# Kernel tuning notes

Measured on AMD Instinct MI355X. Metric: run time of the kernel, lower is better.

Reference implementation:

```python
import jax, jax.numpy as jnp
import numpy as np


def _block_causal_mask(cu_seqlens, seq_len):
    """Boolean [seq_len, seq_len] mask: True = attend (same doc AND causal)."""
    positions = jnp.arange(seq_len)
    # searchsorted(side='right') - 1 maps each position to its document id
    seq_ids = jnp.searchsorted(cu_seqlens, positions, side='right') - 1
    same_seq = seq_ids[:, None] == seq_ids[None, :]
    causal = positions[None, :] <= positions[:, None]
    return same_seq & causal


def setup_inputs() -> dict:
    key = jax.random.key(0)
    kq, kk, kv, kc = jax.random.split(key, 4)
    B, H, S, D = 1, 16, 4096, 128
    q = jax.random.normal(kq, (B, H, S, D), dtype=jnp.float32)
    k = jax.random.normal(kk, (B, H, S, D), dtype=jnp.float32)
    v = jax.random.normal(kv, (B, H, S, D), dtype=jnp.float32)
    # 8 packed documents: interior boundaries are sorted random ints in (0, S)
    inner = jnp.sort(jax.random.randint(kc, (7,), 1, S, dtype=jnp.int64))
    cu_seqlens = jnp.concatenate([
        jnp.zeros((1,), jnp.int64), inner, jnp.full((1,), S, jnp.int64)
    ])
    return {"q": q, "k": k, "v": v, "cu_seqlens": cu_seqlens, "max_seqlen": S}


def reference(q, k, v, cu_seqlens, max_seqlen):
    # q, k, v: [B, H, S, D]; block-diagonal causal SDPA over packed sequences.
    S, D = q.shape[2], q.shape[3]
    scale = 1.0 / jnp.sqrt(jnp.asarray(D, q.dtype))
    allow = _block_causal_mask(cu_seqlens, S)  # [S, S] bool
    scores = jnp.einsum('bhsd,bhtd->bhst', q, k) * scale  # [B, H, S, S]
    neg_inf = jnp.asarray(-jnp.inf, scores.dtype)
    scores = jnp.where(allow[None, None], scores, neg_inf)
    probs = jax.nn.softmax(scores, axis=-1)
    return jnp.einsum('bhst,bhtd->bhsd', probs, v)
```

## Files before the change

kernel.cpp:

```cpp
#include <hip/hip_runtime.h>

typedef float  f32x4  __attribute__((ext_vector_type(4)));
typedef __bf16 bf16x8 __attribute__((ext_vector_type(8)));
typedef unsigned short u16;
typedef u16 u16x8 __attribute__((ext_vector_type(8)));
typedef u16 u16x4 __attribute__((ext_vector_type(4)));
typedef unsigned u32x4 __attribute__((ext_vector_type(4)));

#define HEADS 16
#define DIM   128
#define QT    64
#define KTILE 64
#define PSTR  72
#define KSTR  136
#define VSTR  68

__device__ __forceinline__ u16 f2bf(float f) {
    unsigned u = __builtin_bit_cast(unsigned, f);
    u += 0x7FFFu + ((u >> 16) & 1u);
    return (u16)(u >> 16);
}

__device__ __forceinline__ void dma16(const void* g, void* l) {
    auto* gp = (const __attribute__((address_space(1))) unsigned*)(uintptr_t)g;
    auto* lp = (__attribute__((address_space(3))) unsigned*)(uintptr_t)l;
    __builtin_amdgcn_global_load_lds(gp, lp, 16, 0, 0);
}

__device__ __forceinline__ unsigned cvtpk(float lo, float hi) {
    unsigned r;
    asm("v_cvt_pk_bf16_f32 %0, %1, %2" : "=v"(r) : "v"(lo), "v"(hi));
    return r;
}

__global__ __launch_bounds__(256) void prep_kv(
    const float* __restrict__ K, const float* __restrict__ V,
    u16* __restrict__ KB, u16* __restrict__ VB, int S)
{
    __shared__ __align__(16) u16 T[128 * 72];
    int nt = S >> 6;
    int tile = blockIdx.x % nt, h = blockIdx.x / nt;
    int t = threadIdx.x;
    long tb = (long)(h * nt + tile) * 8192;

    const float* ksrc = K + ((long)(h * S + tile * 64)) * DIM;
#pragma unroll
    for (int it = 0; it < 4; ++it) {
        int idx = t + it * 256;
        int g = idx & 15, r = idx >> 4;
        const float* src = ksrc + (long)r * DIM + g * 8;
        f32x4 a = *(const f32x4*)src;
        f32x4 b = *(const f32x4*)(src + 4);
        u16x8 o;
        o[0]=f2bf(a[0]); o[1]=f2bf(a[1]); o[2]=f2bf(a[2]); o[3]=f2bf(a[3]);
        o[4]=f2bf(b[0]); o[5]=f2bf(b[1]); o[6]=f2bf(b[2]); o[7]=f2bf(b[3]);
        *(u16x8*)&KB[tb + r * 128 + ((g ^ (r & 7)) << 3)] = o;
    }

    int col4 = (t & 31) * 4;
    int row  = t >> 5;
    const float* vsrc = V + ((long)(h * S + tile * 64)) * DIM;
#pragma unroll
    for (int it = 0; it < 8; ++it) {
        int k = row + it * 8;
        f32x4 x = *(const f32x4*)(vsrc + (long)k * DIM + col4);
        T[(col4 + 0) * 72 + k] = f2bf(x[0]);
        T[(col4 + 1) * 72 + k] = f2bf(x[1]);
        T[(col4 + 2) * 72 + k] = f2bf(x[2]);
        T[(col4 + 3) * 72 + k] = f2bf(x[3]);
    }
    __syncthreads();
#pragma unroll
    for (int it = 0; it < 4; ++it) {
        int idx = t + it * 256;
        int d = idx >> 3, g2 = idx & 7;
        u16x8 o = *(const u16x8*)&T[d * 72 + g2 * 8];
        *(u16x8*)&VB[tb + d * 64 + ((g2 ^ (d & 7)) << 3)] = o;
    }
}

__global__ __launch_bounds__(256, 2) void fa_main(
    const float* __restrict__ Q, const u16* __restrict__ KB,
    const u16* __restrict__ VB, const void* __restrict__ cu_raw,
    int n_cu, float* __restrict__ O, int S, int n_qb)
{
    __shared__ __align__(16) u16 Kb[2][64 * 128];
    __shared__ __align__(16) u16 Vt[2][128 * 64];
    __shared__ int cu_s[32];

    const int tid  = threadIdx.x;
    const int wave = tid >> 6, lane = tid & 63;
    const int quad = lane >> 4, l16 = lane & 15;
    const int h  = blockIdx.x & (HEADS - 1);
    const int qb = (n_qb - 1) - (blockIdx.x >> 4);
    const int q0 = qb * QT;

    {
        const int* cu32 = (const int*)cu_raw;
        bool is64 = (cu32[1] == 0);
        for (int t = tid; t < n_cu; t += blockDim.x)
            cu_s[t] = is64 ? (int)((const long long*)cu_raw)[t] : cu32[t];
    }
    __syncthreads();

    const float sc2 = 0.08838834764831845f * 1.4426950408889634f;
    const long hb = (long)h * S * DIM;
    const long hk = (long)h * (S >> 6) * 8192;
    const int qend = q0 + QT;

    const int qi_l = q0 + wave * 16 + l16;
    int qs = 0;
    for (int j = 0; j < n_cu; ++j) if (cu_s[j] <= qi_l) qs = cu_s[j];
    int q0s = 0;
    for (int j = 0; j < n_cu; ++j) if (cu_s[j] <= q0) q0s = cu_s[j];
    const int drange = qi_l - qs;

    bf16x8 qfrag[4];
    {
        const float* qp = Q + hb + (long)qi_l * DIM + quad * 8;
#pragma unroll
        for (int kk = 0; kk < 4; ++kk) {
            f32x4 x = *(const f32x4*)(qp + kk * 32);
            f32x4 y = *(const f32x4*)(qp + kk * 32 + 4);
            u16x8 u;
            u[0]=f2bf(x[0]); u[1]=f2bf(x[1]); u[2]=f2bf(x[2]); u[3]=f2bf(x[3]);
            u[4]=f2bf(y[0]); u[5]=f2bf(y[1]); u[6]=f2bf(y[2]); u[7]=f2bf(y[3]);
            qfrag[kk] = __builtin_bit_cast(bf16x8, u);
        }
    }

    bf16x8 ones;
    {
        u16 ov = (l16 == 0) ? (u16)0x3F80 : (u16)0;
        u16x8 ou;
#pragma unroll
        for (int j = 0; j < 8; ++j) ou[j] = ov;
        ones = __builtin_bit_cast(bf16x8, ou);
    }

    f32x4 acc[9];
#pragma unroll
    for (int dt = 0; dt < 9; ++dt) acc[dt] = (f32x4){0.f, 0.f, 0.f, 0.f};

    const int t0 = (q0s & ~(KTILE - 1)) >> 6;
    const int ntile = (qend >> 6) - t0;
    const u16* ksrc = KB + hk;
    const u16* vsrc = VB + hk;

    {
        long off = (long)t0 * 8192;
#pragma unroll
        for (int c = 0; c < 4; ++c) {
            int ch = wave * 4 + c;
            dma16(ksrc + off + ch * 512 + lane * 8, &Kb[0][ch * 512]);
            dma16(vsrc + off + ch * 512 + lane * 8, &Vt[0][ch * 512]);
        }
    }

    for (int i = 0; i < ntile; ++i) {
        const int cur = i & 1;
        if (i + 1 < ntile) {
            long off = (long)(t0 + i + 1) * 8192;
#pragma unroll
            for (int c = 0; c < 4; ++c) {
                int ch = wave * 4 + c;
                dma16(ksrc + off + ch * 512 + lane * 8, &Kb[cur ^ 1][ch * 512]);
                dma16(vsrc + off + ch * 512 + lane * 8, &Vt[cur ^ 1][ch * 512]);
            }
            asm volatile("s_waitcnt vmcnt(8)" ::: "memory");
        } else {
            asm volatile("s_waitcnt vmcnt(0)" ::: "memory");
        }
        __builtin_amdgcn_s_barrier();

        const int kt = (t0 + i) << 6;
        const u16* kb = &Kb[cur][0];
        const u16* vt = &Vt[cur][0];

        f32x4 sc[4];
        unsigned Ra[4], Rb[4];
        const int base0 = (kt - qs) + quad * 4;
#pragma unroll
        for (int nt = 0; nt < 4; ++nt) sc[nt] = (f32x4){0.f, 0.f, 0.f, 0.f};

#define EXP2N(n)                                                              \
        {                                                                     \
            int b_ = base0 + (n) * 16;                                        \
            float p0 = ((unsigned)(b_ + 0) <= (unsigned)drange)               \
                           ? __builtin_amdgcn_exp2f(sc[n][0] * sc2) : 0.f;    \
            float p1 = ((unsigned)(b_ + 1) <= (unsigned)drange)               \
                           ? __builtin_amdgcn_exp2f(sc[n][1] * sc2) : 0.f;    \
            float p2 = ((unsigned)(b_ + 2) <= (unsigned)drange)               \
                           ? __builtin_amdgcn_exp2f(sc[n][2] * sc2) : 0.f;    \
            float p3 = ((unsigned)(b_ + 3) <= (unsigned)drange)               \
                           ? __builtin_amdgcn_exp2f(sc[n][3] * sc2) : 0.f;    \
            Ra[n] = cvtpk(p0, p1);                                            \
            Rb[n] = cvtpk(p2, p3);                                            \
        }

        __builtin_amdgcn_s_setprio(1);
#pragma unroll
        for (int nt = 0; nt < 4; ++nt) {
#pragma unroll
            for (int kk = 0; kk < 4; ++kk) {
                int row = nt * 16 + l16;
                int g = kk * 4 + quad;
                u16x8 bu = *(const u16x8*)&kb[row * 128 + ((g ^ (row & 7)) << 3)];
                sc[nt] = __builtin_amdgcn_mfma_f32_16x16x32_bf16(
                    __builtin_bit_cast(bf16x8, bu), qfrag[kk], sc[nt], 0, 0, 0);
            }
            if (nt >= 1) EXP2N(nt - 1);
        }
        EXP2N(3);
#undef EXP2N

#pragma unroll
        for (int kk2 = 0; kk2 < 2; ++kk2) {
            unsigned a0 = Ra[2*kk2], a1 = Ra[2*kk2 + 1];
            unsigned b0 = Rb[2*kk2], b1 = Rb[2*kk2 + 1];
            asm("v_permlane32_swap_b32 %0, %1" : "+v"(a0), "+v"(a1));
            asm("v_permlane16_swap_b32 %0, %1" : "+v"(a0), "+v"(a1));
            asm("v_permlane32_swap_b32 %0, %1" : "+v"(b0), "+v"(b1));
            asm("v_permlane16_swap_b32 %0, %1" : "+v"(b0), "+v"(b1));
            u32x4 wv; wv[0] = a0; wv[1] = b0; wv[2] = a1; wv[3] = b1;
            bf16x8 ap = __builtin_bit_cast(bf16x8, wv);

            int g2 = kk2 * 4 + quad;
#pragma unroll
            for (int dt = 0; dt < 8; ++dt) {
                int d = dt * 16 + l16;
                u16x8 bu = *(const u16x8*)&vt[(d << 6) + ((g2 ^ (d & 7)) << 3)];
                acc[dt] = __builtin_amdgcn_mfma_f32_16x16x32_bf16(
                    ap, __builtin_bit_cast(bf16x8, bu), acc[dt], 0, 0, 0);
            }
            acc[8] = __builtin_amdgcn_mfma_f32_16x16x32_bf16(
                ap, ones, acc[8], 0, 0, 0);
        }
        __builtin_amdgcn_s_setprio(0);

        __builtin_amdgcn_s_barrier();
    }

#pragma unroll
    for (int r = 0; r < 4; ++r) {
        float l = __shfl(acc[8][r], (lane & 48), 64);
        int qi = q0 + wave * 16 + quad * 4 + r;
        float inv = 1.f / l;
        float* op = O + hb + (long)qi * DIM + l16;
#pragma unroll
        for (int dt = 0; dt < 8; ++dt)
            op[dt * 16] = acc[dt][r] * inv;
    }
}

__global__ __launch_bounds__(256, 2) void fa_fallback(
    const float* __restrict__ Q, const float* __restrict__ K,
    const float* __restrict__ V, const void* __restrict__ cu_raw,
    int n_cu, float* __restrict__ O, int S)
{
    __shared__ __align__(16) u16 Kb[KTILE * KSTR];
    __shared__ __align__(16) u16 Vt[DIM * VSTR];
    __shared__ __align__(16) u16 Pw[4][16 * PSTR];
    __shared__ int cu_s[32];

    const int tid  = threadIdx.x;
    const int wave = tid >> 6, lane = tid & 63;
    const int quad = lane >> 4, l16 = lane & 15;
    const int q0   = blockIdx.x * QT;
    const int h    = blockIdx.y;
    const int cg = tid & 31, rr = tid >> 5;
    const int dv = tid & 127, hiv = tid >> 7;

    {
        const int* cu32 = (const int*)cu_raw;
        bool is64 = (cu32[1] == 0);
        for (int t = tid; t < n_cu; t += blockDim.x)
            cu_s[t] = is64 ? (int)((const long long*)cu_raw)[t] : cu32[t];
    }
    __syncthreads();

    const long hb = (long)h * S * DIM;
    const float NEG_INF = -__builtin_inff();
    const float scale = 0.08838834764831845f;

    int qstart[4];
#pragma unroll
    for (int r = 0; r < 4; ++r) {
        int qi = q0 + wave * 16 + quad * 4 + r;
        int st = 0;
        for (int j = 0; j < n_cu; ++j) if (cu_s[j] <= qi) st = cu_s[j];
        qstart[r] = st;
    }
    int q0s = 0;
    for (int j = 0; j < n_cu; ++j) if (cu_s[j] <= q0) q0s = cu_s[j];

    bf16x8 qfrag[4];
    {
        const float* qp = Q + hb + (long)(q0 + wave * 16 + l16) * DIM + quad * 8;
#pragma unroll
        for (int kk = 0; kk < 4; ++kk) {
            f32x4 x = *(const f32x4*)(qp + kk * 32);
            f32x4 y = *(const f32x4*)(qp + kk * 32 + 4);
            u16x8 u;
            u[0]=f2bf(x[0]); u[1]=f2bf(x[1]); u[2]=f2bf(x[2]); u[3]=f2bf(x[3]);
            u[4]=f2bf(y[0]); u[5]=f2bf(y[1]); u[6]=f2bf(y[2]); u[7]=f2bf(y[3]);
            qfrag[kk] = __builtin_bit_cast(bf16x8, u);
        }
    }

    f32x4 acc[8];
#pragma unroll
    for (int dt = 0; dt < 8; ++dt) acc[dt] = (f32x4){0.f, 0.f, 0.f, 0.f};
    float m_r[4], l_r[4];
#pragma unroll
    for (int r = 0; r < 4; ++r) { m_r[r] = NEG_INF; l_r[r] = 0.f; }

    for (int kt = q0s & ~(KTILE - 1); kt < q0 + QT; kt += KTILE) {
        __syncthreads();
        {
#pragma unroll
            for (int it = 0; it < 8; ++it) {
                f32x4 kx = *(const f32x4*)(K + hb + (long)(kt + rr + it*8) * DIM + cg*4);
                u16x4 kb4;
                kb4[0]=f2bf(kx[0]); kb4[1]=f2bf(kx[1]);
                kb4[2]=f2bf(kx[2]); kb4[3]=f2bf(kx[3]);
                *(u16x4*)&Kb[(rr + it*8) * KSTR + cg*4] = kb4;
            }
#pragma unroll
            for (int p = 0; p < 8; ++p) {
                int kq = 2*p + hiv;
                const float* vp = V + hb + (long)(kt + kq*4) * DIM + dv;
                u16x4 w;
                w[0]=f2bf(vp[0]); w[1]=f2bf(vp[(long)DIM]);
                w[2]=f2bf(vp[(long)2*DIM]); w[3]=f2bf(vp[(long)3*DIM]);
                *(u16x4*)&Vt[dv * VSTR + kq*4] = w;
            }
        }
        __syncthreads();

        f32x4 sc[4];
#pragma unroll
        for (int nt = 0; nt < 4; ++nt) sc[nt] = (f32x4){0.f, 0.f, 0.f, 0.f};
#pragma unroll
        for (int kk = 0; kk < 4; ++kk)
#pragma unroll
            for (int nt = 0; nt < 4; ++nt) {
                u16x8 bu = *(const u16x8*)&Kb[(nt*16 + l16) * KSTR + kk*32 + quad*8];
                sc[nt] = __builtin_amdgcn_mfma_f32_16x16x32_bf16(
                    qfrag[kk], __builtin_bit_cast(bf16x8, bu), sc[nt], 0, 0, 0);
            }
#pragma unroll
        for (int nt = 0; nt < 4; ++nt) {
            int kj = kt + nt * 16 + l16;
#pragma unroll
            for (int r = 0; r < 4; ++r) {
                int qi = q0 + wave * 16 + quad * 4 + r;
                bool ok = (kj >= qstart[r]) && (kj <= qi);
                sc[nt][r] = ok ? sc[nt][r] * scale : NEG_INF;
            }
        }
        float mnew[4], alpha[4], rsum[4];
#pragma unroll
        for (int r = 0; r < 4; ++r) {
            float tm = fmaxf(fmaxf(sc[0][r], sc[1][r]), fmaxf(sc[2][r], sc[3][r]));
#pragma unroll
            for (int off = 1; off < 16; off <<= 1)
                tm = fmaxf(tm, __shfl_xor(tm, off, 64));
            float mn = fmaxf(m_r[r], tm);
            mnew[r]  = mn;
            alpha[r] = (mn == NEG_INF) ? 1.f : __expf(m_r[r] - mn);
            rsum[r]  = 0.f;
        }
#pragma unroll
        for (int nt = 0; nt < 4; ++nt)
#pragma unroll
            for (int r = 0; r < 4; ++r) {
                float pv = (sc[nt][r] == NEG_INF) ? 0.f : __expf(sc[nt][r] - mnew[r]);
                sc[nt][r] = pv;
                rsum[r] += pv;
            }
#pragma unroll
        for (int r = 0; r < 4; ++r) {
            float s = rsum[r];
#pragma unroll
            for (int off = 1; off < 16; off <<= 1) s += __shfl_xor(s, off, 64);
            l_r[r] = l_r[r] * alpha[r] + s;
            m_r[r] = mnew[r];
        }
#pragma unroll
        for (int dt = 0; dt < 8; ++dt)
#pragma unroll
            for (int r = 0; r < 4; ++r) acc[dt][r] *= alpha[r];

#pragma unroll
        for (int nt = 0; nt < 4; ++nt)
#pragma unroll
            for (int r = 0; r < 4; ++r)
                Pw[wave][(quad*4 + r) * PSTR + ((nt ^ quad) * 16 + l16)] = f2bf(sc[nt][r]);

#pragma unroll
        for (int kk2 = 0; kk2 < 2; ++kk2) {
            int colx = (kk2*32 + quad*8) ^ ((l16 >> 2) << 4);
            u16x8 au = *(const u16x8*)&Pw[wave][l16 * PSTR + colx];
            bf16x8 ap = __builtin_bit_cast(bf16x8, au);
#pragma unroll
            for (int dt = 0; dt < 8; ++dt) {
                int base = (dt*16 + l16) * VSTR + kk2*32 + quad*8;
                u16x4 lo = *(const u16x4*)&Vt[base];
                u16x4 hi = *(const u16x4*)&Vt[base + 4];
                u16x8 bu;
                bu[0]=lo[0]; bu[1]=lo[1]; bu[2]=lo[2]; bu[3]=lo[3];
                bu[4]=hi[0]; bu[5]=hi[1]; bu[6]=hi[2]; bu[7]=hi[3];
                acc[dt] = __builtin_amdgcn_mfma_f32_16x16x32_bf16(
                    ap, __builtin_bit_cast(bf16x8, bu), acc[dt], 0, 0, 0);
            }
        }
    }

#pragma unroll
    for (int r = 0; r < 4; ++r) {
        int qi = q0 + wave * 16 + quad * 4 + r;
        float inv = 1.f / l_r[r];
        float* op = O + hb + (long)qi * DIM + l16;
#pragma unroll
        for (int dt = 0; dt < 8; ++dt)
            op[dt * 16] = acc[dt][r] * inv;
    }
}

extern "C" void kernel_launch(void* const* d_in, const int* in_sizes, int n_in,
                              void* d_out, int out_size, void* d_ws, size_t ws_size,
                              hipStream_t stream) {
    const float* q = (const float*)d_in[0];
    const float* k = (const float*)d_in[1];
    const float* v = (const float*)d_in[2];
    const void* cu = d_in[3];
    int n_cu = in_sizes[3];
    int S = in_sizes[0] / (HEADS * DIM);
    size_t perMat = (size_t)HEADS * S * 256;
    if (ws_size >= 2 * perMat) {
        u16* KB = (u16*)d_ws;
        u16* VB = (u16*)((char*)d_ws + perMat);
        prep_kv<<<dim3(HEADS * (S >> 6)), 256, 0, stream>>>(k, v, KB, VB, S);
        int n_qb = S / QT;
        fa_main<<<dim3(n_qb * HEADS), 256, 0, stream>>>(
            q, KB, VB, cu, n_cu, (float*)d_out, S, n_qb);
    } else {
        fa_fallback<<<dim3(S / QT, HEADS), 256, 0, stream>>>(
            q, k, v, cu, n_cu, (float*)d_out, S);
    }
}
```

Baseline: 172.0 us.

## Single-buffer V via register staging, skip masked tiles, raise occupancy to three

V tile prefetch now goes through registers into a single LDS buffer that is written after the compute barrier, which cuts LDS usage so launch bounds can allow three blocks per CU. The ones-vector MFMA for the row sum is replaced by a scalar per-lane sum reduced with shuffles, and waves skip whole K tiles or 16-row subtiles that lie entirely outside their document/causal range. The cost is extra register pressure from vreg staging, an added wait and LDS store per tile, and divergence-driven imbalance across waves in a block.

```diff
diff --git a/kernel.cpp b/kernel.cpp
--- a/kernel.cpp
+++ b/kernel.cpp
@@ -25,6 +25,12 @@
     auto* gp = (const __attribute__((address_space(1))) unsigned*)(uintptr_t)g;
     auto* lp = (__attribute__((address_space(3))) unsigned*)(uintptr_t)l;
     __builtin_amdgcn_global_load_lds(gp, lp, 16, 0, 0);
+}
+
+__device__ __forceinline__ u32x4 gload16(const void* p) {
+    u32x4 d;
+    asm volatile("global_load_dwordx4 %0, %1, off" : "=v"(d) : "v"(p) : "memory");
+    return d;
 }
 
 __device__ __forceinline__ unsigned cvtpk(float lo, float hi) {
@@ -79,13 +85,13 @@
     }
 }
 
-__global__ __launch_bounds__(256, 2) void fa_main(
+__global__ __launch_bounds__(256, 3) void fa_main(
     const float* __restrict__ Q, const u16* __restrict__ KB,
     const u16* __restrict__ VB, const void* __restrict__ cu_raw,
     int n_cu, float* __restrict__ O, int S, int n_qb)
 {
     __shared__ __align__(16) u16 Kb[2][64 * 128];
-    __shared__ __align__(16) u16 Vt[2][128 * 64];
+    __shared__ __align__(16) u16 Vt[128 * 64];
     __shared__ int cu_s[32];
 
     const int tid  = threadIdx.x;
@@ -114,6 +120,9 @@
     int q0s = 0;
     for (int j = 0; j < n_cu; ++j) if (cu_s[j] <= q0) q0s = cu_s[j];
     const int drange = qi_l - qs;
+
+    const int wqmin = __builtin_amdgcn_readfirstlane(qs);
+    const int wqmax = q0 + wave * 16 + 15;
 
     bf16x8 qfrag[4];
     {
@@ -129,18 +138,10 @@
         }
     }
 
-    bf16x8 ones;
-    {
-        u16 ov = (l16 == 0) ? (u16)0x3F80 : (u16)0;
-        u16x8 ou;
-#pragma unroll
-        for (int j = 0; j < 8; ++j) ou[j] = ov;
-        ones = __builtin_bit_cast(bf16x8, ou);
-    }
-
-    f32x4 acc[9];
-#pragma unroll
-    for (int dt = 0; dt < 9; ++dt) acc[dt] = (f32x4){0.f, 0.f, 0.f, 0.f};
+    f32x4 acc[8];
+#pragma unroll
+    for (int dt = 0; dt < 8; ++dt) acc[dt] = (f32x4){0.f, 0.f, 0.f, 0.f};
+    float lsum = 0.f;
 
     const int t0 = (q0s & ~(KTILE - 1)) >> 6;
     const int ntile = (qend >> 6) - t0;
@@ -153,97 +154,113 @@
         for (int c = 0; c < 4; ++c) {
             int ch = wave * 4 + c;
             dma16(ksrc + off + ch * 512 + lane * 8, &Kb[0][ch * 512]);
-            dma16(vsrc + off + ch * 512 + lane * 8, &Vt[0][ch * 512]);
+            dma16(vsrc + off + ch * 512 + lane * 8, &Vt[ch * 512]);
         }
     }
 
     for (int i = 0; i < ntile; ++i) {
         const int cur = i & 1;
+        u32x4 vreg[4];
         if (i + 1 < ntile) {
             long off = (long)(t0 + i + 1) * 8192;
+            const u16* vsp = vsrc + off + tid * 8;
+#pragma unroll
+            for (int c = 0; c < 4; ++c)
+                vreg[c] = gload16(vsp + c * 2048);
 #pragma unroll
             for (int c = 0; c < 4; ++c) {
                 int ch = wave * 4 + c;
                 dma16(ksrc + off + ch * 512 + lane * 8, &Kb[cur ^ 1][ch * 512]);
-                dma16(vsrc + off + ch * 512 + lane * 8, &Vt[cur ^ 1][ch * 512]);
             }
             asm volatile("s_waitcnt vmcnt(8)" ::: "memory");
         } else {
             asm volatile("s_waitcnt vmcnt(0)" ::: "memory");
         }
+        asm volatile("s_waitcnt lgkmcnt(0)" ::: "memory");
         __builtin_amdgcn_s_barrier();
 
         const int kt = (t0 + i) << 6;
-        const u16* kb = &Kb[cur][0];
-        const u16* vt = &Vt[cur][0];
-
-        f32x4 sc[4];
-        unsigned Ra[4], Rb[4];
-        const int base0 = (kt - qs) + quad * 4;
-#pragma unroll
-        for (int nt = 0; nt < 4; ++nt) sc[nt] = (f32x4){0.f, 0.f, 0.f, 0.f};
+        if (kt <= wqmax && kt + KTILE > wqmin) {
+            const u16* kb = &Kb[cur][0];
+
+            f32x4 sc[4];
+            unsigned Ra[4], Rb[4];
+            const int base0 = (kt - qs) + quad * 4;
+#pragma unroll
+            for (int nt = 0; nt < 4; ++nt) sc[nt] = (f32x4){0.f, 0.f, 0.f, 0.f};
 
 #define EXP2N(n)                                                              \
-        {                                                                     \
-            int b_ = base0 + (n) * 16;                                        \
-            float p0 = ((unsigned)(b_ + 0) <= (unsigned)drange)               \
-                           ? __builtin_amdgcn_exp2f(sc[n][0] * sc2) : 0.f;    \
-            float p1 = ((unsigned)(b_ + 1) <= (unsigned)drange)               \
-                           ? __builtin_amdgcn_exp2f(sc[n][1] * sc2) : 0.f;    \
-            float p2 = ((unsigned)(b_ + 2) <= (unsigned)drange)               \
-                           ? __builtin_amdgcn_exp2f(sc[n][2] * sc2) : 0.f;    \
-            float p3 = ((unsigned)(b_ + 3) <= (unsigned)drange)               \
-                           ? __builtin_amdgcn_exp2f(sc[n][3] * sc2) : 0.f;    \
-            Ra[n] = cvtpk(p0, p1);                                            \
-            Rb[n] = cvtpk(p2, p3);                                            \
-        }
-
-        __builtin_amdgcn_s_setprio(1);
-#pragma unroll
-        for (int nt = 0; nt < 4; ++nt) {
-#pragma unroll
-            for (int kk = 0; kk < 4; ++kk) {
-                int row = nt * 16 + l16;
-                int g = kk * 4 + quad;
-                u16x8 bu = *(const u16x8*)&kb[row * 128 + ((g ^ (row & 7)) << 3)];
-                sc[nt] = __builtin_amdgcn_mfma_f32_16x16x32_bf16(
-                    __builtin_bit_cast(bf16x8, bu), qfrag[kk], sc[nt], 0, 0, 0);
-            }
-            if (nt >= 1) EXP2N(nt - 1);
-        }
-        EXP2N(3);
+            {                                                                 \
+                int b_ = base0 + (n) * 16;                                    \
+                float p0 = ((unsigned)(b_ + 0) <= (unsigned)drange)           \
+                               ? __builtin_amdgcn_exp2f(sc[n][0] * sc2) : 0.f;\
+                float p1 = ((unsigned)(b_ + 1) <= (unsigned)drange)           \
+                               ? __builtin_amdgcn_exp2f(sc[n][1] * sc2) : 0.f;\
+                float p2 = ((unsigned)(b_ + 2) <= (unsigned)drange)           \
+                               ? __builtin_amdgcn_exp2f(sc[n][2] * sc2) : 0.f;\
+                float p3 = ((unsigned)(b_ + 3) <= (unsigned)drange)           \
+                               ? __builtin_amdgcn_exp2f(sc[n][3] * sc2) : 0.f;\
+                lsum += (p0 + p1) + (p2 + p3);                                \
+                Ra[n] = cvtpk(p0, p1);                                        \
+                Rb[n] = cvtpk(p2, p3);                                        \
+            }
+
+            __builtin_amdgcn_s_setprio(1);
+#pragma unroll
+            for (int nt = 0; nt < 4; ++nt) {
+                if (kt + nt * 16 <= wqmax) {
+#pragma unroll
+                    for (int kk = 0; kk < 4; ++kk) {
+                        int row = nt * 16 + l16;
+                        int g = kk * 4 + quad;
+                        u16x8 bu = *(const u16x8*)&kb[row * 128 + ((g ^ (row & 7)) << 3)];
+                        sc[nt] = __builtin_amdgcn_mfma_f32_16x16x32_bf16(
+                            __builtin_bit_cast(bf16x8, bu), qfrag[kk], sc[nt], 0, 0, 0);
+                    }
+                }
+                if (nt >= 1) EXP2N(nt - 1);
+            }
+            EXP2N(3);
 #undef EXP2N
 
 #pragma unroll
-        for (int kk2 = 0; kk2 < 2; ++kk2) {
-            unsigned a0 = Ra[2*kk2], a1 = Ra[2*kk2 + 1];
-            unsigned b0 = Rb[2*kk2], b1 = Rb[2*kk2 + 1];
-            asm("v_permlane32_swap_b32 %0, %1" : "+v"(a0), "+v"(a1));
-            asm("v_permlane16_swap_b32 %0, %1" : "+v"(a0), "+v"(a1));
-            asm("v_permlane32_swap_b32 %0, %1" : "+v"(b0), "+v"(b1));
-            asm("v_permlane16_swap_b32 %0, %1" : "+v"(b0), "+v"(b1));
-            u32x4 wv; wv[0] = a0; wv[1] = b0; wv[2] = a1; wv[3] = b1;
-            bf16x8 ap = __builtin_bit_cast(bf16x8, wv);
-
-            int g2 = kk2 * 4 + quad;
-#pragma unroll
-            for (int dt = 0; dt < 8; ++dt) {
-                int d = dt * 16 + l16;
-                u16x8 bu = *(const u16x8*)&vt[(d << 6) + ((g2 ^ (d & 7)) << 3)];
-                acc[dt] = __builtin_amdgcn_mfma_f32_16x16x32_bf16(
-                    ap, __builtin_bit_cast(bf16x8, bu), acc[dt], 0, 0, 0);
-            }
-            acc[8] = __builtin_amdgcn_mfma_f32_16x16x32_bf16(
-                ap, ones, acc[8], 0, 0, 0);
-        }
-        __builtin_amdgcn_s_setprio(0);
+            for (int kk2 = 0; kk2 < 2; ++kk2) {
+                unsigned a0 = Ra[2*kk2], a1 = Ra[2*kk2 + 1];
+                unsigned b0 = Rb[2*kk2], b1 = Rb[2*kk2 + 1];
+                asm("v_permlane32_swap_b32 %0, %1" : "+v"(a0), "+v"(a1));
+                asm("v_permlane16_swap_b32 %0, %1" : "+v"(a0), "+v"(a1));
+                asm("v_permlane32_swap_b32 %0, %1" : "+v"(b0), "+v"(b1));
+                asm("v_permlane16_swap_b32 %0, %1" : "+v"(b0), "+v"(b1));
+                u32x4 wv; wv[0] = a0; wv[1] = b0; wv[2] = a1; wv[3] = b1;
+                bf16x8 ap = __builtin_bit_cast(bf16x8, wv);
+
+                int g2 = kk2 * 4 + quad;
+#pragma unroll
+                for (int dt = 0; dt < 8; ++dt) {
+                    int d = dt * 16 + l16;
+                    u16x8 bu = *(const u16x8*)&Vt[(d << 6) + ((g2 ^ (d & 7)) << 3)];
+                    acc[dt] = __builtin_amdgcn_mfma_f32_16x16x32_bf16(
+                        ap, __builtin_bit_cast(bf16x8, bu), acc[dt], 0, 0, 0);
+                }
+            }
+            __builtin_amdgcn_s_setprio(0);
+        }
 
         __builtin_amdgcn_s_barrier();
-    }
-
+        if (i + 1 < ntile) {
+            asm volatile("s_waitcnt vmcnt(4)" ::: "memory");
+#pragma unroll
+            for (int c = 0; c < 4; ++c)
+                *(u32x4*)&Vt[tid * 8 + c * 2048] = vreg[c];
+        }
+    }
+
+    float lred = lsum;
+    lred += __shfl_xor(lred, 16, 64);
+    lred += __shfl_xor(lred, 32, 64);
 #pragma unroll
     for (int r = 0; r < 4; ++r) {
-        float l = __shfl(acc[8][r], (lane & 48), 64);
+        float l = __shfl(lred, quad * 4 + r, 64);
         int qi = q0 + wave * 16 + quad * 4 + r;
         float inv = 1.f / l;
         float* op = O + hb + (long)qi * DIM + l16;
```

Result: slower. 177.8 us (+3.4%).

## Drop K/V double buffering to single-buffer LDS and raise occupancy to 4 blocks

Applied to the files above, without the earlier changes.

Replaces the double-buffered K/V shared-memory tiles with a single buffer, halving LDS use to 32KB per block, and raises launch bounds to 4 blocks per CU. The shared cu_seqlens staging and its barrier are removed; each thread now reads the boundaries directly from global memory. The aim is to hide load latency through more resident waves instead of software prefetch. In exchange each tile now loads synchronously with a full vmcnt(0) wait, and the tighter register budget for 4 blocks may cause spills given the 9 accumulators plus Q fragments.

```diff
diff --git a/kernel.cpp b/kernel.cpp
--- a/kernel.cpp
+++ b/kernel.cpp
@@ -79,14 +79,13 @@
     }
 }
 
-__global__ __launch_bounds__(256, 2) void fa_main(
+__global__ __launch_bounds__(256, 4) void fa_main(
     const float* __restrict__ Q, const u16* __restrict__ KB,
     const u16* __restrict__ VB, const void* __restrict__ cu_raw,
     int n_cu, float* __restrict__ O, int S, int n_qb)
 {
-    __shared__ __align__(16) u16 Kb[2][64 * 128];
-    __shared__ __align__(16) u16 Vt[2][128 * 64];
-    __shared__ int cu_s[32];
+    __shared__ __align__(16) u16 Kb[64 * 128];
+    __shared__ __align__(16) u16 Vt[128 * 64];
 
     const int tid  = threadIdx.x;
     const int wave = tid >> 6, lane = tid & 63;
@@ -95,24 +94,23 @@
     const int qb = (n_qb - 1) - (blockIdx.x >> 4);
     const int q0 = qb * QT;
 
-    {
-        const int* cu32 = (const int*)cu_raw;
-        bool is64 = (cu32[1] == 0);
-        for (int t = tid; t < n_cu; t += blockDim.x)
-            cu_s[t] = is64 ? (int)((const long long*)cu_raw)[t] : cu32[t];
-    }
-    __syncthreads();
-
     const float sc2 = 0.08838834764831845f * 1.4426950408889634f;
     const long hb = (long)h * S * DIM;
     const long hk = (long)h * (S >> 6) * 8192;
     const int qend = q0 + QT;
 
     const int qi_l = q0 + wave * 16 + l16;
-    int qs = 0;
-    for (int j = 0; j < n_cu; ++j) if (cu_s[j] <= qi_l) qs = cu_s[j];
-    int q0s = 0;
-    for (int j = 0; j < n_cu; ++j) if (cu_s[j] <= q0) q0s = cu_s[j];
+    int qs = 0, q0s = 0;
+    {
+        const int* cu32 = (const int*)cu_raw;
+        const long long* cu64 = (const long long*)cu_raw;
+        bool is64 = (cu32[1] == 0);
+        for (int j = 0; j < n_cu; ++j) {
+            int v = is64 ? (int)cu64[j] : cu32[j];
+            if (v <= qi_l) qs = v;
+            if (v <= q0)   q0s = v;
+        }
+    }
     const int drange = qi_l - qs;
 
     bf16x8 qfrag[4];
@@ -147,35 +145,20 @@
     const u16* ksrc = KB + hk;
     const u16* vsrc = VB + hk;
 
-    {
-        long off = (long)t0 * 8192;
-#pragma unroll
-        for (int c = 0; c < 4; ++c) {
-            int ch = wave * 4 + c;
-            dma16(ksrc + off + ch * 512 + lane * 8, &Kb[0][ch * 512]);
-            dma16(vsrc + off + ch * 512 + lane * 8, &Vt[0][ch * 512]);
-        }
-    }
-
     for (int i = 0; i < ntile; ++i) {
-        const int cur = i & 1;
-        if (i + 1 < ntile) {
-            long off = (long)(t0 + i + 1) * 8192;
+        {
+            long off = (long)(t0 + i) * 8192;
 #pragma unroll
             for (int c = 0; c < 4; ++c) {
                 int ch = wave * 4 + c;
-                dma16(ksrc + off + ch * 512 + lane * 8, &Kb[cur ^ 1][ch * 512]);
-                dma16(vsrc + off + ch * 512 + lane * 8, &Vt[cur ^ 1][ch * 512]);
-            }
-            asm volatile("s_waitcnt vmcnt(8)" ::: "memory");
-        } else {
-            asm volatile("s_waitcnt vmcnt(0)" ::: "memory");
-        }
+                dma16(ksrc + off + ch * 512 + lane * 8, &Kb[ch * 512]);
+                dma16(vsrc + off + ch * 512 + lane * 8, &Vt[ch * 512]);
+            }
+        }
+        asm volatile("s_waitcnt vmcnt(0)" ::: "memory");
         __builtin_amdgcn_s_barrier();
 
         const int kt = (t0 + i) << 6;
-        const u16* kb = &Kb[cur][0];
-        const u16* vt = &Vt[cur][0];
 
         f32x4 sc[4];
         unsigned Ra[4], Rb[4];
@@ -205,7 +188,7 @@
             for (int kk = 0; kk < 4; ++kk) {
                 int row = nt * 16 + l16;
                 int g = kk * 4 + quad;
-                u16x8 bu = *(const u16x8*)&kb[row * 128 + ((g ^ (row & 7)) << 3)];
+                u16x8 bu = *(const u16x8*)&Kb[row * 128 + ((g ^ (row & 7)) << 3)];
                 sc[nt] = __builtin_amdgcn_mfma_f32_16x16x32_bf16(
                     __builtin_bit_cast(bf16x8, bu), qfrag[kk], sc[nt], 0, 0, 0);
             }
@@ -229,7 +212,7 @@
 #pragma unroll
             for (int dt = 0; dt < 8; ++dt) {
                 int d = dt * 16 + l16;
-                u16x8 bu = *(const u16x8*)&vt[(d << 6) + ((g2 ^ (d & 7)) << 3)];
+                u16x8 bu = *(const u16x8*)&Vt[(d << 6) + ((g2 ^ (d & 7)) << 3)];
                 acc[dt] = __builtin_amdgcn_mfma_f32_16x16x32_bf16(
                     ap, __builtin_bit_cast(bf16x8, bu), acc[dt], 0, 0, 0);
             }
```

Result: slower. 176.5 us (+2.6%).
